# Kernel optimization log

Hardware: AMD Instinct MI355X
Metric: run time of the kernel (lower is better)

Reference implementation:

```python
import jax, jax.numpy as jnp
import numpy as np

B, L, H, V = 64, 8, 4096, 50257


def setup_inputs() -> dict:
    key = jax.random.key(0)
    ks = jax.random.split(key, 5)
    return {
        "embedding": jax.random.normal(ks[0], (V, H), jnp.float32) * 0.02,
        "hidden_states": jax.random.normal(ks[1], (B, L, H), jnp.float32),
        "output_position": 7,  # scalar index of the position to sample from
        "temperatures": jax.random.uniform(ks[2], (B,), jnp.float32, 0.5, 1.5),
        "top_ps": jax.random.uniform(ks[3], (B,), jnp.float32, 0.7, 1.0),
        "tops_ks": jax.random.randint(ks[4], (B,), 1, 64),  # top-k in [1,64)
        "embedding_bias": jnp.zeros((V,), jnp.float32),
    }


def reference(embedding, hidden_states, output_position, temperatures, top_ps, tops_ks, embedding_bias):
    # select the output position: [B, H]
    h = hidden_states[:, output_position, :]
    # logits GEMM against tied embedding: [B, V]
    logits = jnp.einsum("bh,vh->bv", h, embedding) + embedding_bias[None, :]
    logits = logits / temperatures[:, None]
    probs = jax.nn.softmax(logits.astype(jnp.float32), axis=-1)

    # descending sort of probabilities
    order = jnp.argsort(-probs, axis=-1)                       # [B, V]
    probs_sort = jnp.take_along_axis(probs, order, axis=-1)    # [B, V]

    # top-p mask: exclusive cumulative sum exceeding top_p
    cum = jnp.cumsum(probs_sort, axis=-1)
    topp_mask = (cum - probs_sort) > top_ps[:, None]
    # top-k mask: rank >= k
    ranks = jnp.arange(V, dtype=tops_ks.dtype)[None, :]
    topk_mask = ranks >= tops_ks[:, None]

    probs_sort = jnp.where(topp_mask | topk_mask, 0.0, probs_sort)
    probs_sort = probs_sort / jnp.sum(probs_sort, axis=-1, keepdims=True)

    # scatter back to original vocab order via inverse permutation
    inv = jnp.argsort(order, axis=-1)
    probs_final = jnp.take_along_axis(probs_sort, inv, axis=-1)  # [B, V]

    # multinomial sampling (1 sample per row)
    logp = jnp.where(probs_final > 0, jnp.log(jnp.maximum(probs_final, 1e-38)), -jnp.inf)
    next_token_ids = jax.random.categorical(jax.random.key(42), logp, axis=-1)
    return next_token_ids
```

## Files before the change

### kernel.cpp

```cpp
#include <hip/hip_runtime.h>
#include <stdint.h>
#include <float.h>
#include <limits.h>


typedef __bf16 bf16x8 __attribute__((ext_vector_type(8)));
typedef float  f32x4  __attribute__((ext_vector_type(4)));

#define BN 64
#define BK 64

__device__ __forceinline__ unsigned short f2bf_rn(float x) {
    uint32_t u = __float_as_uint(x);
    u += 0x7FFFu + ((u >> 16) & 1u);
    return (unsigned short)(u >> 16);
}
__device__ __forceinline__ float bf2f(unsigned short h) {
    return __uint_as_float(((uint32_t)h) << 16);
}

__global__ __launch_bounds__(256) void logits_mfma(
    const float* __restrict__ emb,
    const float* __restrict__ hs,
    const int*   __restrict__ pos_p,
    const float* __restrict__ temps,
    const float* __restrict__ bias,
    float*       __restrict__ out,
    int V, int H, int L)
{
    __shared__ unsigned short sAhi[64 * 64];
    __shared__ unsigned short sAlo[64 * 64];
    __shared__ unsigned short sBhi[64 * 64];
    __shared__ unsigned short sBlo[64 * 64];

    const int tid = threadIdx.x;
    const int v0  = blockIdx.x * BN;
    const int pos = pos_p[0];

    const int srow = tid >> 3;
    const int scol = (tid & 7) * 8;

    const int lane  = tid & 63;
    const int w     = tid >> 6;
    const int rbase = (w >> 1) * 32;
    const int cbase = (w & 1) * 32;

    int offA[2][2], offB[2][2];
#pragma unroll
    for (int i = 0; i < 2; ++i) {
        const int ra = rbase + 16 * i + (lane & 15);
        const int rb = cbase + 16 * i + (lane & 15);
#pragma unroll
        for (int ks = 0; ks < 2; ++ks) {
            const int ke = 32 * ks + (lane >> 4) * 8;
            offA[i][ks] = ra * 64 + (ke ^ ((ra & 7) * 8));
            offB[i][ks] = rb * 64 + (ke ^ ((rb & 7) * 8));
        }
    }

    f32x4 acc[2][2];
#pragma unroll
    for (int i = 0; i < 2; ++i)
#pragma unroll
        for (int j = 0; j < 2; ++j)
            acc[i][j] = (f32x4){0.f, 0.f, 0.f, 0.f};

    float4 pB[2][2], pA[2][2];

    auto issue = [&](int k0) {
#pragma unroll
        for (int p = 0; p < 2; ++p) {
            const int row = srow + 32 * p;
            const int v   = v0 + row;
            if (v < V) {
                const float* bp = emb + (size_t)v * H + (k0 + scol);
                pB[p][0] = *(const float4*)bp;
                pB[p][1] = *(const float4*)(bp + 4);
            } else {
                pB[p][0] = make_float4(0.f, 0.f, 0.f, 0.f);
                pB[p][1] = make_float4(0.f, 0.f, 0.f, 0.f);
            }
            const float* ap = hs + ((size_t)row * L + pos) * H + (k0 + scol);
            pA[p][0] = *(const float4*)ap;
            pA[p][1] = *(const float4*)(ap + 4);
        }
    };

    auto stage = [&]() {
#pragma unroll
        for (int p = 0; p < 2; ++p) {
            const int row = srow + 32 * p;
            const int off = row * 64 + (scol ^ ((row & 7) * 8));

            float fb[8] = { pB[p][0].x, pB[p][0].y, pB[p][0].z, pB[p][0].w,
                            pB[p][1].x, pB[p][1].y, pB[p][1].z, pB[p][1].w };
            float fa[8] = { pA[p][0].x, pA[p][0].y, pA[p][0].z, pA[p][0].w,
                            pA[p][1].x, pA[p][1].y, pA[p][1].z, pA[p][1].w };
            uint32_t bh[4], bl[4], ah[4], al[4];
#pragma unroll
            for (int q = 0; q < 4; ++q) {
                const unsigned short h0 = f2bf_rn(fb[2*q]);
                const unsigned short h1 = f2bf_rn(fb[2*q+1]);
                const unsigned short l0 = f2bf_rn(fb[2*q]   - bf2f(h0));
                const unsigned short l1 = f2bf_rn(fb[2*q+1] - bf2f(h1));
                bh[q] = (uint32_t)h0 | ((uint32_t)h1 << 16);
                bl[q] = (uint32_t)l0 | ((uint32_t)l1 << 16);
                const unsigned short g0 = f2bf_rn(fa[2*q]);
                const unsigned short g1 = f2bf_rn(fa[2*q+1]);
                const unsigned short m0 = f2bf_rn(fa[2*q]   - bf2f(g0));
                const unsigned short m1 = f2bf_rn(fa[2*q+1] - bf2f(g1));
                ah[q] = (uint32_t)g0 | ((uint32_t)g1 << 16);
                al[q] = (uint32_t)m0 | ((uint32_t)m1 << 16);
            }
            *(uint4*)&sBhi[off] = make_uint4(bh[0], bh[1], bh[2], bh[3]);
            *(uint4*)&sBlo[off] = make_uint4(bl[0], bl[1], bl[2], bl[3]);
            *(uint4*)&sAhi[off] = make_uint4(ah[0], ah[1], ah[2], ah[3]);
            *(uint4*)&sAlo[off] = make_uint4(al[0], al[1], al[2], al[3]);
        }
    };

    issue(0);
    for (int k0 = 0; k0 < H; k0 += BK) {
        __syncthreads();
        stage();
        __syncthreads();
        if (k0 + BK < H) issue(k0 + BK);

        bf16x8 fah[2][2], fal[2][2];
#pragma unroll
        for (int i = 0; i < 2; ++i)
#pragma unroll
            for (int ks = 0; ks < 2; ++ks) {
                fah[i][ks] = *(const bf16x8*)&sAhi[offA[i][ks]];
                fal[i][ks] = *(const bf16x8*)&sAlo[offA[i][ks]];
            }
#pragma unroll
        for (int j = 0; j < 2; ++j) {
            bf16x8 fbh[2], fbl[2];
#pragma unroll
            for (int ks = 0; ks < 2; ++ks) {
                fbh[ks] = *(const bf16x8*)&sBhi[offB[j][ks]];
                fbl[ks] = *(const bf16x8*)&sBlo[offB[j][ks]];
            }
#pragma unroll
            for (int i = 0; i < 2; ++i)
#pragma unroll
                for (int ks = 0; ks < 2; ++ks) {
                    acc[i][j] = __builtin_amdgcn_mfma_f32_16x16x32_bf16(
                        fal[i][ks], fbh[ks], acc[i][j], 0, 0, 0);
                    acc[i][j] = __builtin_amdgcn_mfma_f32_16x16x32_bf16(
                        fah[i][ks], fbl[ks], acc[i][j], 0, 0, 0);
                    acc[i][j] = __builtin_amdgcn_mfma_f32_16x16x32_bf16(
                        fah[i][ks], fbh[ks], acc[i][j], 0, 0, 0);
                }
        }
    }

#pragma unroll
    for (int i = 0; i < 2; ++i)
#pragma unroll
        for (int j = 0; j < 2; ++j) {
            const int vv = v0 + cbase + 16 * j + (lane & 15);
            if (vv < V) {
                const float bv = bias[vv];
#pragma unroll
                for (int r = 0; r < 4; ++r) {
                    const int b = rbase + 16 * i + (lane >> 4) * 4 + r;
                    out[(size_t)b * V + vv] = (acc[i][j][r] + bv) / temps[b];
                }
            }
        }
}

__device__ __forceinline__ uint32_t rotl32(uint32_t x, int d) {
    return (x << d) | (x >> (32 - d));
}

__device__ float jax_gumbel(uint32_t flat) {
    const uint32_t k0 = 0u, k1 = 42u;
    const uint32_t ks[3] = { k0, k1, k0 ^ k1 ^ 0x1BD11BDAu };
    uint32_t x0 = 0u   + ks[0];
    uint32_t x1 = flat + ks[1];
    const int rot[2][4] = { {13, 15, 26, 6}, {17, 29, 16, 24} };
#pragma unroll
    for (int r = 0; r < 5; ++r) {
        const int* rr = rot[r & 1];
#pragma unroll
        for (int j = 0; j < 4; ++j) {
            x0 += x1;
            x1 = rotl32(x1, rr[j]);
            x1 ^= x0;
        }
        x0 += ks[(r + 1) % 3];
        x1 += ks[(r + 2) % 3] + (uint32_t)(r + 1);
    }
    const uint32_t bits = x0 ^ x1;
    const uint32_t fb = (bits >> 9) | 0x3F800000u;
    const float f = __uint_as_float(fb) - 1.0f;
    const float tiny = 1.17549435e-38f;
    float u = __fadd_rn(__fmul_rn(f, 1.0f), tiny);
    u = fmaxf(tiny, u);
    const float l1 = logf(u);
    return -logf(-l1);
}

#define NBINS 4096
#define CAP   2048
#define NKEEP 64

__global__ __launch_bounds__(256) void sample_kernel(
    const float* __restrict__ logits,
    const float* __restrict__ top_ps,
    const int*   __restrict__ top_ks,
    int*         __restrict__ out_ids,
    int V)
{
    const int b = blockIdx.x;
    const int tid = threadIdx.x;
    const float* row = logits + (size_t)b * V;

    __shared__ float swred[4];
    __shared__ int   bins[NBINS];
    __shared__ int   schunk[256];
    __shared__ int   sThrBin, sCnt, sMkeep;
    __shared__ float cval[CAP];
    __shared__ int   cidx[CAP];
    __shared__ float tval[NKEEP];
    __shared__ int   tidxs[NKEEP];

    float m = -INFINITY;
    for (int k = tid; k < V; k += 256) m = fmaxf(m, row[k]);
#pragma unroll
    for (int o = 32; o > 0; o >>= 1) m = fmaxf(m, __shfl_xor(m, o, 64));
    if ((tid & 63) == 0) swred[tid >> 6] = m;
    __syncthreads();
    m = fmaxf(fmaxf(swred[0], swred[1]), fmaxf(swred[2], swred[3]));

    for (int k = tid; k < NBINS; k += 256) bins[k] = 0;
    if (tid == 0) sCnt = 0;
    __syncthreads();

    float s = 0.f;
    for (int k = tid; k < V; k += 256) {
        const float x = row[k];
        s += expf(x - m);
        const float g = m - x;
        int bin = (int)(g * 256.0f);
        if (bin >= NBINS) bin = NBINS - 1;
        atomicAdd(&bins[bin], 1);
    }
#pragma unroll
    for (int o = 32; o > 0; o >>= 1) s += __shfl_xor(s, o, 64);
    __syncthreads();
    if ((tid & 63) == 0) swred[tid >> 6] = s;

    int csum = 0;
#pragma unroll
    for (int k = 0; k < NBINS / 256; ++k) csum += bins[tid * (NBINS / 256) + k];
    schunk[tid] = csum;
    __syncthreads();
    s = swred[0] + swred[1] + swred[2] + swred[3];
    if (tid == 0) {
        int cum = 0, chunk = 255;
        for (int c = 0; c < 256; ++c) {
            if (cum + schunk[c] >= NKEEP) { chunk = c; break; }
            cum += schunk[c];
        }
        int t = NBINS - 1;
        const int base = chunk * (NBINS / 256);
        for (int k = base; k < base + NBINS / 256; ++k) {
            cum += bins[k];
            if (cum >= NKEEP) { t = k; break; }
        }
        sThrBin = t;
    }
    __syncthreads();
    const int thrBin = sThrBin;

    for (int k = tid; k < V; k += 256) {
        const float x = row[k];
        const float g = m - x;
        int bin = (int)(g * 256.0f);
        if (bin >= NBINS) bin = NBINS - 1;
        if (bin <= thrBin) {
            const int p = atomicAdd(&sCnt, 1);
            if (p < CAP) { cval[p] = x; cidx[p] = k; }
        }
    }
    __syncthreads();
    const int C = min(sCnt, CAP);

    for (int i = tid; i < C; i += 256) {
        const float vi = cval[i];
        const int   ii = cidx[i];
        int rank = 0;
        for (int j = 0; j < C; ++j) {
            const float vj = cval[j];
            const int   ij = cidx[j];
            rank += (vj > vi) || (vj == vi && ij < ii);
        }
        if (rank < NKEEP) { tval[rank] = vi; tidxs[rank] = ii; }
    }
    __syncthreads();

    if (tid == 0) {
        const float pb = top_ps[b];
        const int   kk = top_ks[b];
        const int   nk = min(NKEEP, C);
        float cum = 0.f;
        int mk = 0;
        for (int r = 0; r < nk; ++r) {
            const float pr = expf(tval[r] - m) / s;
            cum += pr;
            const float excl = cum - pr;
            if (excl > pb || r >= kk) break;
            ++mk;
        }
        sMkeep = (mk > 0) ? mk : 1;
    }
    __syncthreads();
    const int mkeep = sMkeep;

    if (tid < 64) {
        float sc = -INFINITY;
        int vid = INT_MAX;
        if (tid < mkeep) {
            const int v = tidxs[tid];
            vid = v;
            sc = tval[tid] + jax_gumbel((uint32_t)b * (uint32_t)V + (uint32_t)v);
        }
#pragma unroll
        for (int o = 32; o > 0; o >>= 1) {
            const float os = __shfl_xor(sc, o, 64);
            const int   ov = __shfl_xor(vid, o, 64);
            if (os > sc || (os == sc && ov < vid)) { sc = os; vid = ov; }
        }
        if (tid == 0) out_ids[b] = vid;
    }
}

extern "C" void kernel_launch(void* const* d_in, const int* in_sizes, int n_in,
                              void* d_out, int out_size, void* d_ws, size_t ws_size,
                              hipStream_t stream)
{
    const float* emb   = (const float*)d_in[0];
    const float* hs    = (const float*)d_in[1];
    const int*   pos   = (const int*)d_in[2];
    const float* temps = (const float*)d_in[3];
    const float* tps   = (const float*)d_in[4];
    const int*   tks   = (const int*)d_in[5];
    const float* bias  = (const float*)d_in[6];

    const int B = in_sizes[3];
    const int V = in_sizes[6];
    const int H = (int)((long long)in_sizes[0] / V);
    const int L = (int)((long long)in_sizes[1] / ((long long)B * H));

    float* logits = (float*)d_ws;

    const int nblk = (V + BN - 1) / BN;
    logits_mfma<<<nblk, 256, 0, stream>>>(emb, hs, pos, temps, bias,
                                          logits, V, H, L);

    sample_kernel<<<B, 256, 0, stream>>>(logits, tps, tks, (int*)d_out, V);
}
```

Before: 361.1 us.

## Pre-split hidden states into bf16 hi/lo once, double-buffer embedding tiles

Adds a prep kernel that gathers the selected position of the hidden states and converts it once into bf16 hi/lo pairs, stored in MFMA fragment order in workspace. The GEMM kernel then reads A fragments straight from global memory (cached in L2) instead of having every block reload and re-split fp32 A through LDS. The embedding tiles are now double-buffered in LDS, so one barrier per k-step is dropped and the split of the next tile runs after the MFMAs. The cost is an extra kernel launch and direct global reads of A fragments inside the inner loop, which may add latency.

```diff
diff --git a/kernel.cpp b/kernel.cpp
--- a/kernel.cpp
+++ b/kernel.cpp
@@ -10,53 +10,119 @@
 #define BN 64
 #define BK 64
 
-__device__ __forceinline__ unsigned short f2bf_rn(float x) {
-    uint32_t u = __float_as_uint(x);
-    u += 0x7FFFu + ((u >> 16) & 1u);
-    return (unsigned short)(u >> 16);
-}
-__device__ __forceinline__ float bf2f(unsigned short h) {
-    return __uint_as_float(((uint32_t)h) << 16);
+__device__ __forceinline__ void split8(const float* f, uint4& hi, uint4& lo) {
+    bf16x8 vh, vl;
+#pragma unroll
+    for (int e = 0; e < 8; ++e) {
+        const __bf16 h = (__bf16)f[e];
+        vh[e] = h;
+        vl[e] = (__bf16)(f[e] - (float)h);
+    }
+    hi = __builtin_bit_cast(uint4, vh);
+    lo = __builtin_bit_cast(uint4, vl);
+}
+
+__global__ __launch_bounds__(256) void prep_h(
+    const float* __restrict__ hs, const int* __restrict__ pos_p,
+    unsigned short* __restrict__ Ahi, unsigned short* __restrict__ Alo,
+    int H, int L)
+{
+    const int pos = pos_p[0];
+    const int tid = blockIdx.x * 256 + threadIdx.x;
+    const int b     = tid >> 8;
+    const int kbase = (tid & 255) * 16;
+    const float* src = hs + ((size_t)b * L + pos) * H + kbase;
+    float f[16];
+    *(float4*)&f[0]  = *(const float4*)(src);
+    *(float4*)&f[4]  = *(const float4*)(src + 4);
+    *(float4*)&f[8]  = *(const float4*)(src + 8);
+    *(float4*)&f[12] = *(const float4*)(src + 12);
+
+    const int r16 = b >> 4, ll = b & 15;
+    const int kc  = kbase >> 5;
+    const int lh0 = (kbase >> 3) & 3;
+#pragma unroll
+    for (int c = 0; c < 2; ++c) {
+        uint4 hi, lo;
+        split8(f + 8 * c, hi, lo);
+        const size_t dst = ((size_t)(r16 * 128 + kc) * 64 + (lh0 + c) * 16 + ll) * 8;
+        *(uint4*)&Ahi[dst] = hi;
+        *(uint4*)&Alo[dst] = lo;
+    }
 }
 
 __global__ __launch_bounds__(256) void logits_mfma(
     const float* __restrict__ emb,
-    const float* __restrict__ hs,
-    const int*   __restrict__ pos_p,
+    const unsigned short* __restrict__ Ahi,
+    const unsigned short* __restrict__ Alo,
     const float* __restrict__ temps,
     const float* __restrict__ bias,
     float*       __restrict__ out,
-    int V, int H, int L)
+    int V, int H)
 {
-    __shared__ unsigned short sAhi[64 * 64];
-    __shared__ unsigned short sAlo[64 * 64];
-    __shared__ unsigned short sBhi[64 * 64];
-    __shared__ unsigned short sBlo[64 * 64];
+    __shared__ unsigned short sBhi[2][64 * 64];
+    __shared__ unsigned short sBlo[2][64 * 64];
 
     const int tid = threadIdx.x;
     const int v0  = blockIdx.x * BN;
-    const int pos = pos_p[0];
-
-    const int srow = tid >> 3;
-    const int scol = (tid & 7) * 8;
+
+    const int brow = tid >> 2;
+    const int bcol = (tid & 3) * 16;
 
     const int lane  = tid & 63;
     const int w     = tid >> 6;
     const int rbase = (w >> 1) * 32;
     const int cbase = (w & 1) * 32;
 
-    int offA[2][2], offB[2][2];
-#pragma unroll
-    for (int i = 0; i < 2; ++i) {
-        const int ra = rbase + 16 * i + (lane & 15);
-        const int rb = cbase + 16 * i + (lane & 15);
+    int offB[2][2];
+#pragma unroll
+    for (int j = 0; j < 2; ++j) {
+        const int rb = cbase + 16 * j + (lane & 15);
 #pragma unroll
         for (int ks = 0; ks < 2; ++ks) {
             const int ke = 32 * ks + (lane >> 4) * 8;
-            offA[i][ks] = ra * 64 + (ke ^ ((ra & 7) * 8));
-            offB[i][ks] = rb * 64 + (ke ^ ((rb & 7) * 8));
-        }
-    }
+            offB[j][ks] = rb * 64 + (ke ^ ((rb & 7) * 8));
+        }
+    }
+    const int wswz  = (brow & 7) * 8;
+    const int woff0 = brow * 64 + (bcol ^ wswz);
+    const int woff1 = brow * 64 + ((bcol + 8) ^ wswz);
+
+    size_t abase[2];
+#pragma unroll
+    for (int i = 0; i < 2; ++i)
+        abase[i] = (size_t)((w >> 1) * 2 + i) * 65536
+                 + (size_t)(lane >> 4) * 128 + (size_t)(lane & 15) * 8;
+
+    const int vglob = v0 + brow;
+    const float* bsrc = emb + (size_t)vglob * H + bcol;
+
+    float4 pf[4];
+    auto issueB = [&](int k0) {
+        if (vglob < V) {
+#pragma unroll
+            for (int q = 0; q < 4; ++q)
+                pf[q] = *(const float4*)(bsrc + k0 + 4 * q);
+        } else {
+#pragma unroll
+            for (int q = 0; q < 4; ++q)
+                pf[q] = make_float4(0.f, 0.f, 0.f, 0.f);
+        }
+    };
+    auto stageB = [&](int buf) {
+        float f[16];
+        *(float4*)&f[0]  = pf[0];
+        *(float4*)&f[4]  = pf[1];
+        *(float4*)&f[8]  = pf[2];
+        *(float4*)&f[12] = pf[3];
+        uint4 h0, l0, h1, l1;
+        split8(f,     h0, l0);
+        split8(f + 8, h1, l1);
+        *(uint4*)&sBhi[buf][woff0] = h0;
+        *(uint4*)&sBlo[buf][woff0] = l0;
+        *(uint4*)&sBhi[buf][woff1] = h1;
+        *(uint4*)&sBlo[buf][woff1] = l1;
+    };
 
     f32x4 acc[2][2];
 #pragma unroll
@@ -65,82 +131,31 @@
         for (int j = 0; j < 2; ++j)
             acc[i][j] = (f32x4){0.f, 0.f, 0.f, 0.f};
 
-    float4 pB[2][2], pA[2][2];
-
-    auto issue = [&](int k0) {
-#pragma unroll
-        for (int p = 0; p < 2; ++p) {
-            const int row = srow + 32 * p;
-            const int v   = v0 + row;
-            if (v < V) {
-                const float* bp = emb + (size_t)v * H + (k0 + scol);
-                pB[p][0] = *(const float4*)bp;
-                pB[p][1] = *(const float4*)(bp + 4);
-            } else {
-                pB[p][0] = make_float4(0.f, 0.f, 0.f, 0.f);
-                pB[p][1] = make_float4(0.f, 0.f, 0.f, 0.f);
-            }
-            const float* ap = hs + ((size_t)row * L + pos) * H + (k0 + scol);
-            pA[p][0] = *(const float4*)ap;
-            pA[p][1] = *(const float4*)(ap + 4);
-        }
-    };
-
-    auto stage = [&]() {
-#pragma unroll
-        for (int p = 0; p < 2; ++p) {
-            const int row = srow + 32 * p;
-            const int off = row * 64 + (scol ^ ((row & 7) * 8));
-
-            float fb[8] = { pB[p][0].x, pB[p][0].y, pB[p][0].z, pB[p][0].w,
-                            pB[p][1].x, pB[p][1].y, pB[p][1].z, pB[p][1].w };
-            float fa[8] = { pA[p][0].x, pA[p][0].y, pA[p][0].z, pA[p][0].w,
-                            pA[p][1].x, pA[p][1].y, pA[p][1].z, pA[p][1].w };
-            uint32_t bh[4], bl[4], ah[4], al[4];
-#pragma unroll
-            for (int q = 0; q < 4; ++q) {
-                const unsigned short h0 = f2bf_rn(fb[2*q]);
-                const unsigned short h1 = f2bf_rn(fb[2*q+1]);
-                const unsigned short l0 = f2bf_rn(fb[2*q]   - bf2f(h0));
-                const unsigned short l1 = f2bf_rn(fb[2*q+1] - bf2f(h1));
-                bh[q] = (uint32_t)h0 | ((uint32_t)h1 << 16);
-                bl[q] = (uint32_t)l0 | ((uint32_t)l1 << 16);
-                const unsigned short g0 = f2bf_rn(fa[2*q]);
-                const unsigned short g1 = f2bf_rn(fa[2*q+1]);
-                const unsigned short m0 = f2bf_rn(fa[2*q]   - bf2f(g0));
-                const unsigned short m1 = f2bf_rn(fa[2*q+1] - bf2f(g1));
-                ah[q] = (uint32_t)g0 | ((uint32_t)g1 << 16);
-                al[q] = (uint32_t)m0 | ((uint32_t)m1 << 16);
-            }
-            *(uint4*)&sBhi[off] = make_uint4(bh[0], bh[1], bh[2], bh[3]);
-            *(uint4*)&sBlo[off] = make_uint4(bl[0], bl[1], bl[2], bl[3]);
-            *(uint4*)&sAhi[off] = make_uint4(ah[0], ah[1], ah[2], ah[3]);
-            *(uint4*)&sAlo[off] = make_uint4(al[0], al[1], al[2], al[3]);
-        }
-    };
-
-    issue(0);
+    issueB(0);
+    stageB(0);
+    int cur = 0;
     for (int k0 = 0; k0 < H; k0 += BK) {
         __syncthreads();
-        stage();
-        __syncthreads();
-        if (k0 + BK < H) issue(k0 + BK);
-
+        const bool more = (k0 + BK) < H;
+        if (more) issueB(k0 + BK);
+
+        const int kc = k0 >> 5;
         bf16x8 fah[2][2], fal[2][2];
 #pragma unroll
         for (int i = 0; i < 2; ++i)
 #pragma unroll
             for (int ks = 0; ks < 2; ++ks) {
-                fah[i][ks] = *(const bf16x8*)&sAhi[offA[i][ks]];
-                fal[i][ks] = *(const bf16x8*)&sAlo[offA[i][ks]];
+                const size_t ai = abase[i] + (size_t)(kc + ks) * 512;
+                fah[i][ks] = *(const bf16x8*)&Ahi[ai];
+                fal[i][ks] = *(const bf16x8*)&Alo[ai];
             }
 #pragma unroll
         for (int j = 0; j < 2; ++j) {
             bf16x8 fbh[2], fbl[2];
 #pragma unroll
             for (int ks = 0; ks < 2; ++ks) {
-                fbh[ks] = *(const bf16x8*)&sBhi[offB[j][ks]];
-                fbl[ks] = *(const bf16x8*)&sBlo[offB[j][ks]];
+                fbh[ks] = *(const bf16x8*)&sBhi[cur][offB[j][ks]];
+                fbl[ks] = *(const bf16x8*)&sBlo[cur][offB[j][ks]];
             }
 #pragma unroll
             for (int i = 0; i < 2; ++i)
@@ -154,6 +169,8 @@
                         fah[i][ks], fbh[ks], acc[i][j], 0, 0, 0);
                 }
         }
+        if (more) stageB(cur ^ 1);
+        cur ^= 1;
     }
 
 #pragma unroll
@@ -356,11 +373,15 @@
     const int H = (int)((long long)in_sizes[0] / V);
     const int L = (int)((long long)in_sizes[1] / ((long long)B * H));
 
-    float* logits = (float*)d_ws;
+    float*          logits = (float*)d_ws;
+    unsigned short* Ahi    = (unsigned short*)((char*)d_ws + (16u << 20));
+    unsigned short* Alo    = Ahi + (size_t)B * H;
+
+    prep_h<<<(B * H) / (16 * 256), 256, 0, stream>>>(hs, pos, Ahi, Alo, H, L);
 
     const int nblk = (V + BN - 1) / BN;
-    logits_mfma<<<nblk, 256, 0, stream>>>(emb, hs, pos, temps, bias,
-                                          logits, V, H, L);
+    logits_mfma<<<nblk, 256, 0, stream>>>(emb, Ahi, Alo, temps, bias,
+                                          logits, V, H);
 
     sample_kernel<<<B, 256, 0, stream>>>(logits, tps, tks, (int*)d_out, V);
 }
```

New measurement: 354.7 us. About the same (-1.8%).
